# Performance work log

Measured on AMD Instinct MI355X. Metric: run time of the kernel, lower is better.

## Reference

```python
import jax, jax.numpy as jnp
import numpy as np

N_Q = 4
DEPTH = 6
DIM = 16  # 2**N_Q

# ---- fixed `design` dict (forward arg in the torch module; fixed here so the
# gate sequence is static, exercising every gate branch) ----
_K1 = ['x', 'y', 'z']
_K2 = ['H', 'Px', 'Py', 'Pz', 'CNot', 'CZ', 'Tof', 'CSwap']
DESIGN = {}
for _l in range(DEPTH):
    for _n in range(N_Q):
        DESIGN[str(_l) + str(_n) + '0'] = ((_l + _n) % 2 == 0)
        DESIGN[str(_l) + str(_n) + '1'] = _K1[(_l + _n) % 3]
        DESIGN[str(_l) + str(_n) + '2'] = _K2[(_l * N_Q + _n) % 8]

# ---- elementary gate matrices (numpy, build-time) ----
_H = np.array([[1, 1], [1, -1]], np.complex64) / np.sqrt(2.0)
_X = np.array([[0, 1], [1, 0]], np.complex64)
_Y = np.array([[0, -1j], [1j, 0]], np.complex64)
_Z = np.array([[1, 0], [0, -1]], np.complex64)
_CNOT = np.eye(4, dtype=np.complex64)[[0, 1, 3, 2]]
_CZ = np.diag(np.array([1, 1, 1, -1], np.complex64))
_TOF = np.eye(8, dtype=np.complex64)[[0, 1, 2, 3, 4, 5, 7, 6]]
_CSWAP = np.eye(8, dtype=np.complex64)[[0, 1, 2, 3, 4, 6, 5, 7]]


def _embed(gate, wires):
    # Embed a 2^k x 2^k gate acting on `wires` (wire 0 = most-significant bit,
    # PennyLane convention) into a full 16x16 unitary.
    k = len(wires)
    U = np.zeros((DIM, DIM), np.complex64)
    for i in range(DIM):
        bits = [(i >> (N_Q - 1 - q)) & 1 for q in range(N_Q)]
        sub_in = 0
        for w in wires:
            sub_in = (sub_in << 1) | bits[w]
        for sub_out in range(2 ** k):
            amp = gate[sub_out, sub_in]
            if amp != 0:
                ob = list(bits)
                for j, w in enumerate(wires):
                    ob[w] = (sub_out >> (k - 1 - j)) & 1
                o = 0
                for q in range(N_Q):
                    o = (o << 1) | ob[q]
                U[o, i] += amp
    return jnp.asarray(U)


# ---- static op list: ('fix', U16) | ('rot', kind, wire, angle_source) ----
_G1 = {'H': _H, 'Px': _X, 'Py': _Y, 'Pz': _Z}
OPS = [('fix', _embed(_H, [q])) for q in range(N_Q)]  # initial Hadamards
for _l in range(DEPTH):
    for _n in range(N_Q):
        if DESIGN[str(_l) + str(_n) + '0']:
            OPS.append(('rot', 'y', _n, ('x', _n)))  # RY(input feature)
        OPS.append(('rot', DESIGN[str(_l) + str(_n) + '1'], _n, ('w', _l, _n)))
        g = DESIGN[str(_l) + str(_n) + '2']
        if g in _G1:
            OPS.append(('fix', _embed(_G1[g], [_n])))
        elif g == 'CNot':
            OPS.append(('fix', _embed(_CNOT, [_n, (_n + 1) % N_Q])))
        elif g == 'CZ':
            OPS.append(('fix', _embed(_CZ, [_n, (_n + 1) % N_Q])))
        elif g == 'Tof':
            OPS.append(('fix', _embed(_TOF, [_n, (_n + 1) % N_Q, (_n + 2) % N_Q])))
        elif g == 'CSwap':
            OPS.append(('fix', _embed(_CSWAP, [_n, (_n + 1) % N_Q, (_n + 2) % N_Q])))


def _rot_mat(kind, th):
    # th: (B,) real angles -> (B,2,2) complex64 rotation matrices
    half = 0.5 * th
    c = jnp.cos(half).astype(jnp.complex64)
    s = jnp.sin(half).astype(jnp.complex64)
    if kind == 'x':
        m = [[c, (-1j) * s], [(-1j) * s, c]]
    elif kind == 'y':
        m = [[c, -s], [s, c]]
    else:  # 'z'
        e = jnp.exp((-1j) * half.astype(jnp.complex64))
        z = jnp.zeros_like(e)
        m = [[e, z], [z, jnp.conj(e)]]
    return jnp.stack([jnp.stack(m[0], -1), jnp.stack(m[1], -1)], -2)


def _apply_1q(state, M, q):
    # state: (B,16) complex, M: (B,2,2) complex, single-qubit gate on wire q
    B = state.shape[0]
    s = state.reshape(B, 2 ** q, 2, 2 ** (N_Q - 1 - q))
    s = jnp.einsum('bij,bajc->baic', M, s)
    return s.reshape(B, DIM)


def _run(state, x, w, adjoint):
    # adjoint: reversed gate order, negated rotation angles; all fixed gates
    # here (H, Paulis, CNOT, CZ, Toffoli, CSWAP) are Hermitian => self-adjoint.
    sign = -1.0 if adjoint else 1.0
    B = state.shape[0]
    for op in (reversed(OPS) if adjoint else OPS):
        if op[0] == 'fix':
            state = jnp.einsum('ij,bj->bi', op[1], state)
        else:
            _, kind, wire, src = op
            th = x[:, src[1]] if src[0] == 'x' else jnp.broadcast_to(w[src[1], src[2]], (B,))
            state = _apply_1q(state, _rot_mat(kind, sign * th), wire)
    return state


def _forward(x1, x2, q_params):
    w = q_params.reshape(DEPTH, N_Q)
    B = x1.shape[0]
    state = jnp.zeros((B, DIM), jnp.complex64).at[:, 0].set(1.0)
    state = _run(state, x1, w, False)   # quantum_net(x1, w)
    state = _run(state, x2, w, True)    # adjoint(quantum_net)(x2, w)
    a = state[:, 0]                     # probs[0] = |<0...0|psi>|^2
    return a.real ** 2 + a.imag ** 2


def setup_inputs():
    key = jax.random.key(0)
    k1, k2, k3 = jax.random.split(key, 3)
    B = 262144
    return {
        'x1': jax.random.normal(k1, (B, N_Q), jnp.float32),
        'x2': jax.random.normal(k2, (B, N_Q), jnp.float32),
        'q_params': jax.random.normal(k3, (DEPTH * N_Q,), jnp.float32),
    }


def reference(x1, x2, q_params):
    return _forward(x1, x2, q_params)
```

## Files before the change

kernel.cpp:

```cpp
#include <hip/hip_runtime.h>
#include <math.h>


#define DEVI static __device__ __forceinline__

typedef float f2 __attribute__((ext_vector_type(2)));

DEVI f2 sp(float x) { f2 r; r.x = x; r.y = x; return r; }
DEVI f2 mk(float x, float y) { f2 r; r.x = x; r.y = y; return r; }
DEVI f2 fm(f2 a, f2 b, f2 c) { return __builtin_elementwise_fma(a, b, c); }
DEVI f2 nI(f2 a) { f2 r; r.x = a.y;  r.y = -a.x; return r; }
DEVI f2 pI(f2 a) { f2 r; r.x = -a.y; r.y = a.x;  return r; }
DEVI f2 cmulc(f2 a, f2 g, f2 ig) { return fm(sp(a.y), ig, sp(a.x) * g); }


template<int Q> DEVI void gX(f2* v) {
  constexpr int m = 1 << (3 - Q);
#pragma unroll
  for (int i = 0; i < 16; ++i) if (!(i & m)) {
    const int j = i | m; f2 t = v[i]; v[i] = v[j]; v[j] = t;
  }
}

template<int Q> DEVI void gRY(f2* v, float c, float s) {
  constexpr int m = 1 << (3 - Q);
  const f2 C = sp(c), S = sp(s), NS = sp(-s);
#pragma unroll
  for (int i = 0; i < 16; ++i) if (!(i & m)) {
    const int j = i | m;
    f2 a = v[i], b = v[j];
    v[i] = fm(b, NS, a * C);
    v[j] = fm(b, C,  a * S);
  }
}

template<int Q> DEVI void gRX(f2* v, float c, float s) {
  constexpr int m = 1 << (3 - Q);
  const f2 C = sp(c), S = sp(s);
#pragma unroll
  for (int i = 0; i < 16; ++i) if (!(i & m)) {
    const int j = i | m;
    f2 a = v[i], b = v[j];
    v[i] = fm(nI(b), S, a * C);
    v[j] = fm(nI(a), S, b * C);
  }
}

template<int Q> DEVI void gRZ(f2* v, float c, float s) {
  constexpr int m = 1 << (3 - Q);
  const f2 g0 = mk(c, -s), ig0 = mk(s, c);
  const f2 g1 = mk(c,  s), ig1 = mk(-s, c);
#pragma unroll
  for (int i = 0; i < 16; ++i) {
    f2 a = v[i];
    v[i] = (i & m) ? cmulc(a, g1, ig1) : cmulc(a, g0, ig0);
  }
}

template<int Q> DEVI void gHRX(f2* v, f2 Em, f2 Ep, f2 iEm, f2 iEp) {
  constexpr int m = 1 << (3 - Q);
#pragma unroll
  for (int i = 0; i < 16; ++i) if (!(i & m)) {
    const int j = i | m;
    f2 a = v[i], b = v[j];
    f2 t = a + b, u = a - b;
    v[i] = cmulc(t, Em, iEm);
    v[j] = cmulc(u, Ep, iEp);
  }
}

template<int Q> DEVI void gHRZ(f2* v, f2 Em, f2 Ep, f2 iEm, f2 iEp) {
  constexpr int m = 1 << (3 - Q);
#pragma unroll
  for (int i = 0; i < 16; ++i) if (!(i & m)) {
    const int j = i | m;
    f2 a = v[i], b = v[j];
    f2 p = cmulc(a, Em, iEm), q = cmulc(b, Ep, iEp);
    v[i] = p + q;
    v[j] = p - q;
  }
}

template<int Q> DEVI void gYRZ(f2* v, f2 G1, f2 G2, f2 iG1, f2 iG2) {
  constexpr int m = 1 << (3 - Q);
#pragma unroll
  for (int i = 0; i < 16; ++i) if (!(i & m)) {
    const int j = i | m;
    f2 a = v[i], b = v[j];
    v[i] = cmulc(b, G1, iG1);
    v[j] = cmulc(a, G2, iG2);
  }
}

template<int Q> DEVI void gYRX(f2* v, float c, float s) {
  constexpr int m = 1 << (3 - Q);
  const f2 C = sp(c), S = sp(s), NS = sp(-s);
#pragma unroll
  for (int i = 0; i < 16; ++i) if (!(i & m)) {
    const int j = i | m;
    f2 a = v[i], b = v[j];
    v[i] = fm(nI(b), C, a * NS);
    v[j] = fm(pI(a), C, b * S);
  }
}

template<int Q> DEVI void gZRX(f2* v, float c, float s) {
  constexpr int m = 1 << (3 - Q);
  const f2 C = sp(c), S = sp(s), NC = sp(-c);
#pragma unroll
  for (int i = 0; i < 16; ++i) if (!(i & m)) {
    const int j = i | m;
    f2 a = v[i], b = v[j];
    v[i] = fm(nI(b), S, a * C);
    v[j] = fm(pI(a), S, b * NC);
  }
}

template<int Q> DEVI void gZRZ(f2* v, float c, float s) {
  constexpr int m = 1 << (3 - Q);
  const f2 g0 = mk(c, -s),  ig0 = mk(s, c);
  const f2 g1 = mk(-c, -s), ig1 = mk(s, -c);
#pragma unroll
  for (int i = 0; i < 16; ++i) {
    f2 a = v[i];
    v[i] = (i & m) ? cmulc(a, g1, ig1) : cmulc(a, g0, ig0);
  }
}

template<int Q> DEVI void gZRY(f2* v, float c, float s) {
  constexpr int m = 1 << (3 - Q);
  const f2 C = sp(c), NS = sp(-s), NC = sp(-c);
#pragma unroll
  for (int i = 0; i < 16; ++i) if (!(i & m)) {
    const int j = i | m;
    f2 a = v[i], b = v[j];
    v[i] = fm(b, NS, a * C);
    v[j] = fm(b, NC, a * NS);
  }
}

template<int Q> DEVI void gHRY(f2* v, float c, float s) {
  constexpr int m = 1 << (3 - Q);
  const float K = 0.70710678118654752440f;
  const float al = K * (c + s), be = K * (c - s);
  const f2 AL = sp(al), BE = sp(be), NAL = sp(-al);
#pragma unroll
  for (int i = 0; i < 16; ++i) if (!(i & m)) {
    const int j = i | m;
    f2 a = v[i], b = v[j];
    v[i] = fm(b, BE,  a * AL);
    v[j] = fm(b, NAL, a * BE);
  }
}

template<int Q> DEVI void gYRY(f2* v, float c, float s) {
  constexpr int m = 1 << (3 - Q);
  const f2 C = sp(c), S = sp(s), NS = sp(-s);
#pragma unroll
  for (int i = 0; i < 16; ++i) if (!(i & m)) {
    const int j = i | m;
    f2 a = v[i], b = v[j];
    f2 t = fm(b, C, a * S);
    f2 u = fm(b, NS, a * C);
    v[i] = nI(t);
    v[j] = pI(u);
  }
}

template<int A, int B2> DEVI void gCZ(f2* v) {
  constexpr int ma = 1 << (3 - A), mb = 1 << (3 - B2);
#pragma unroll
  for (int i = 0; i < 16; ++i) if ((i & ma) && (i & mb)) v[i] = -v[i];
}

template<int C, int T> DEVI void gCNOT(f2* v) {
  constexpr int mc = 1 << (3 - C), mt = 1 << (3 - T);
#pragma unroll
  for (int i = 0; i < 16; ++i) if ((i & mc) && !(i & mt)) {
    const int j = i | mt; f2 t = v[i]; v[i] = v[j]; v[j] = t;
  }
}

template<int C1, int C2, int T> DEVI void gTOF(f2* v) {
  constexpr int m1 = 1 << (3 - C1), m2 = 1 << (3 - C2), mt = 1 << (3 - T);
#pragma unroll
  for (int i = 0; i < 16; ++i) if ((i & m1) && (i & m2) && !(i & mt)) {
    const int j = i | mt; f2 t = v[i]; v[i] = v[j]; v[j] = t;
  }
}

template<int C, int A, int B2> DEVI void gCSWAP(f2* v) {
  constexpr int mc = 1 << (3 - C), ma = 1 << (3 - A), mb = 1 << (3 - B2);
#pragma unroll
  for (int i = 0; i < 16; ++i) if ((i & mc) && (i & ma) && !(i & mb)) {
    const int j = (i ^ ma) | mb; f2 t = v[i]; v[i] = v[j]; v[j] = t;
  }
}

DEVI void fwd(f2* v, const float* cx, const float* sx,
              const float* cw, const float* sw) {
  const float K = 0.70710678118654752440f;
  const f2 Em0  = mk(K*cw[0], -K*sw[0]), Ep0  = mk(K*cw[0],  K*sw[0]);
  const f2 iEm0 = mk(K*sw[0],  K*cw[0]), iEp0 = mk(-K*sw[0], K*cw[0]);
  const f2 G1   = mk(sw[2], -cw[2]),     G2   = mk(sw[2],  cw[2]);
  const f2 iG1  = mk(cw[2],  sw[2]),     iG2  = mk(-cw[2], sw[2]);
  const f2 Em8  = mk(K*cw[8], -K*sw[8]), Ep8  = mk(K*cw[8],  K*sw[8]);
  const f2 iEm8 = mk(K*sw[8],  K*cw[8]), iEp8 = mk(-K*sw[8], K*cw[8]);
  const float c73  = cx[3]*cw[7]  - sx[3]*sw[7],  s73  = sx[3]*cw[7]  + cx[3]*sw[7];
  const float c102 = cx[2]*cw[10] - sx[2]*sw[10], s102 = sx[2]*cw[10] + cx[2]*sw[10];
  const float c131 = cx[1]*cw[13] - sx[1]*sw[13], s131 = sx[1]*cw[13] + cx[1]*sw[13];
  const float c160 = cx[0]*cw[16] - sx[0]*sw[16], s160 = sx[0]*cw[16] + cx[0]*sw[16];

  gRY<0>(v, cx[0], sx[0]); gHRX<0>(v, Em0, Ep0, iEm0, iEp0);
  gRY<1>(v, cw[1], sw[1]); gX<1>(v);
  gRY<2>(v, cx[2], sx[2]); gYRZ<2>(v, G1, G2, iG1, iG2);
  gZRX<3>(v, cw[3], sw[3]);
  gRY<0>(v, cw[4], sw[4]); gCNOT<0,1>(v);
  gRY<1>(v, cx[1], sx[1]); gRZ<1>(v, cw[5], sw[5]); gCZ<1,2>(v);
  gRX<2>(v, cw[6], sw[6]); gTOF<2,3,0>(v);
  gRY<3>(v, c73, s73);     gCSWAP<3,0,1>(v);
  gRY<0>(v, cx[0], sx[0]); gHRZ<0>(v, Em8, Ep8, iEm8, iEp8);
  gRX<1>(v, cw[9], sw[9]); gX<1>(v);
  gYRY<2>(v, c102, s102);
  gZRZ<3>(v, cw[11], sw[11]);
  gRX<0>(v, cw[12], sw[12]); gCNOT<0,1>(v);
  gRY<1>(v, c131, s131);     gCZ<1,2>(v);
  gRZ<2>(v, cw[14], sw[14]); gTOF<2,3,0>(v);
  gRY<3>(v, cx[3], sx[3]); gRX<3>(v, cw[15], sw[15]); gCSWAP<3,0,1>(v);
  gHRY<0>(v, c160, s160);
  gRZ<1>(v, cw[17], sw[17]); gX<1>(v);
  gRY<2>(v, cx[2], sx[2]); gYRX<2>(v, cw[18], sw[18]);
  gZRY<3>(v, cw[19], sw[19]);
  gRZ<0>(v, cw[20], sw[20]); gCNOT<0,1>(v);
  gRY<1>(v, cx[1], sx[1]); gRX<1>(v, cw[21], sw[21]); gCZ<1,2>(v);
  gRY<2>(v, cw[22], sw[22]); gTOF<2,3,0>(v);
  gRY<3>(v, cx[3], sx[3]); gRZ<3>(v, cw[23], sw[23]); gCSWAP<3,0,1>(v);
}

DEVI float rlane(float v, int l) {
  return __int_as_float(__builtin_amdgcn_readlane(__float_as_int(v), l));
}

__global__ __launch_bounds__(256, 4)
void qsim(const float* __restrict__ x1, const float* __restrict__ x2,
          const float* __restrict__ q, float* __restrict__ out, int B)
{
  const int b = blockIdx.x * blockDim.x + threadIdx.x;
  if (b >= B) return;

  const int lane = threadIdx.x & 63;
  float qv = 0.f;
  if (lane < 24) qv = q[lane];
  float mys, myc;
  __sincosf(0.5f * qv, &mys, &myc);

  float cw[24], sw[24];
#pragma unroll
  for (int k = 0; k < 24; ++k) { cw[k] = rlane(myc, k); sw[k] = rlane(mys, k); }

  const float4 xa = reinterpret_cast<const float4*>(x1)[b];
  const float4 xb = reinterpret_cast<const float4*>(x2)[b];
  float ca[4], sa[4], cb[4], sb[4];
  __sincosf(0.5f * xa.x, &sa[0], &ca[0]);
  __sincosf(0.5f * xa.y, &sa[1], &ca[1]);
  __sincosf(0.5f * xa.z, &sa[2], &ca[2]);
  __sincosf(0.5f * xa.w, &sa[3], &ca[3]);
  __sincosf(0.5f * xb.x, &sb[0], &cb[0]);
  __sincosf(0.5f * xb.y, &sb[1], &cb[1]);
  __sincosf(0.5f * xb.z, &sb[2], &cb[2]);
  __sincosf(0.5f * xb.w, &sb[3], &cb[3]);

  f2 vA[16], vB[16];
#pragma unroll
  for (int i = 0; i < 16; ++i) {
    vA[i] = mk(0.25f, 0.f);
    vB[i] = mk(0.25f, 0.f);
  }

  fwd(vA, ca, sa, cw, sw);
  fwd(vB, cb, sb, cw, sw);

  f2 acc = mk(0.f, 0.f);
#pragma unroll
  for (int i = 0; i < 16; ++i) {
    f2 t1 = mk(vA[i].x, vA[i].y) * sp(vB[i].x);
    f2 t2 = mk(vA[i].y, -vA[i].x) * sp(vB[i].y);
    acc = acc + t1 + t2;
  }
  out[b] = acc.x * acc.x + acc.y * acc.y;
}

extern "C" void kernel_launch(void* const* d_in, const int* in_sizes, int n_in,
                              void* d_out, int out_size, void* d_ws, size_t ws_size,
                              hipStream_t stream) {
  const float* x1 = (const float*)d_in[0];
  const float* x2 = (const float*)d_in[1];
  const float* q  = (const float*)d_in[2];
  float* out = (float*)d_out;
  const int B = in_sizes[0] / 4;
  const int block = 256;
  const int grid = (B + block - 1) / block;
  qsim<<<grid, block, 0, stream>>>(x1, x2, q, out, B);
}
```

Before: 78.66 us.

## Split forward and adjoint circuits across wave halves, combine via cross-lane shuffle

```diff
diff --git a/kernel.cpp b/kernel.cpp
--- a/kernel.cpp
+++ b/kernel.cpp
@@ -241,53 +241,54 @@
   return __int_as_float(__builtin_amdgcn_readlane(__float_as_int(v), l));
 }
 
-__global__ __launch_bounds__(256, 4)
+__global__ __launch_bounds__(256, 6)
 void qsim(const float* __restrict__ x1, const float* __restrict__ x2,
           const float* __restrict__ q, float* __restrict__ out, int B)
 {
-  const int b = blockIdx.x * blockDim.x + threadIdx.x;
-  if (b >= B) return;
-
+  const int t = blockIdx.x * blockDim.x + threadIdx.x;
   const int lane = threadIdx.x & 63;
+  const int half = lane >> 5;
+  const int j = lane & 31;
+  const int e = (t >> 6) * 32 + j;
+  if (e >= B) return;
+
   float qv = 0.f;
   if (lane < 24) qv = q[lane];
   float mys, myc;
   __sincosf(0.5f * qv, &mys, &myc);
-
   float cw[24], sw[24];
 #pragma unroll
   for (int k = 0; k < 24; ++k) { cw[k] = rlane(myc, k); sw[k] = rlane(mys, k); }
 
-  const float4 xa = reinterpret_cast<const float4*>(x1)[b];
-  const float4 xb = reinterpret_cast<const float4*>(x2)[b];
-  float ca[4], sa[4], cb[4], sb[4];
-  __sincosf(0.5f * xa.x, &sa[0], &ca[0]);
-  __sincosf(0.5f * xa.y, &sa[1], &ca[1]);
-  __sincosf(0.5f * xa.z, &sa[2], &ca[2]);
-  __sincosf(0.5f * xa.w, &sa[3], &ca[3]);
-  __sincosf(0.5f * xb.x, &sb[0], &cb[0]);
-  __sincosf(0.5f * xb.y, &sb[1], &cb[1]);
-  __sincosf(0.5f * xb.z, &sb[2], &cb[2]);
-  __sincosf(0.5f * xb.w, &sb[3], &cb[3]);
-
-  f2 vA[16], vB[16];
+  const float4 xv = half ? reinterpret_cast<const float4*>(x2)[e]
+                         : reinterpret_cast<const float4*>(x1)[e];
+  float cx[4], sx[4];
+  __sincosf(0.5f * xv.x, &sx[0], &cx[0]);
+  __sincosf(0.5f * xv.y, &sx[1], &cx[1]);
+  __sincosf(0.5f * xv.z, &sx[2], &cx[2]);
+  __sincosf(0.5f * xv.w, &sx[3], &cx[3]);
+
+  f2 v[16];
+#pragma unroll
+  for (int i = 0; i < 16; ++i) v[i] = mk(0.25f, 0.f);
+
+  fwd(v, cx, sx, cw, sw);
+
+  f2 o[16];
 #pragma unroll
   for (int i = 0; i < 16; ++i) {
-    vA[i] = mk(0.25f, 0.f);
-    vB[i] = mk(0.25f, 0.f);
-  }
-
-  fwd(vA, ca, sa, cw, sw);
-  fwd(vB, cb, sb, cw, sw);
+    o[i].x = __shfl_xor(v[i].x, 32, 64);
+    o[i].y = __shfl_xor(v[i].y, 32, 64);
+  }
 
   f2 acc = mk(0.f, 0.f);
 #pragma unroll
   for (int i = 0; i < 16; ++i) {
-    f2 t1 = mk(vA[i].x, vA[i].y) * sp(vB[i].x);
-    f2 t2 = mk(vA[i].y, -vA[i].x) * sp(vB[i].y);
+    f2 t1 = mk(v[i].x, v[i].y) * sp(o[i].x);
+    f2 t2 = mk(v[i].y, -v[i].x) * sp(o[i].y);
     acc = acc + t1 + t2;
   }
-  out[b] = acc.x * acc.x + acc.y * acc.y;
+  if (!half) out[e] = acc.x * acc.x + acc.y * acc.y;
 }
 
 extern "C" void kernel_launch(void* const* d_in, const int* in_sizes, int n_in,
@@ -299,6 +300,7 @@
   float* out = (float*)d_out;
   const int B = in_sizes[0] / 4;
   const int block = 256;
-  const int grid = (B + block - 1) / block;
+  const long long threads = 2LL * B;
+  const int grid = (int)((threads + block - 1) / block);
   qsim<<<grid, block, 0, stream>>>(x1, x2, q, out, B);
 }
```

After: 84.25 us. 7.1% more time.
